# Performance work log

Measured on AMD Instinct MI355X. Metric: run time of the kernel, lower is better.

Reference implementation:

```python
import jax, jax.numpy as jnp
import numpy as np

B, C_IN, C_OUT, T, R, CO = 8, 64, 64, 32, 32, 32


def setup_inputs() -> dict:
    key = jax.random.key(0)
    ks = jax.random.split(key, 8)
    scale = 1.0 / np.sqrt(C_IN)  # nn.Linear default uniform(-1/sqrt(in), 1/sqrt(in))
    w = lambda k: jax.random.uniform(k, (C_OUT, C_IN), jnp.float32, -scale, scale)
    return {
        "x": jax.random.normal(ks[0], (B, C_IN, T, R, CO), jnp.float32),
        "w_self": w(ks[1]),
        "w_tp": w(ks[2]),
        "w_tm": w(ks[3]),
        "w_rp": w(ks[4]),
        "w_rm": w(ks[5]),
        "w_cp": w(ks[6]),
        "w_cm": w(ks[7]),
    }


def _proj(v, w):
    # v: [B, t, r, c, C_in], w: [C_out, C_in] (nn.Linear layout)
    return jnp.einsum('btrci,oi->btrco', v, w)


def _shift_pad(a, axis, front):
    # pad 1 slice at front (True) or back (False) along `axis` of a 5-D tensor
    pads = [(0, 0)] * 5
    pads[axis] = (1, 0) if front else (0, 1)
    return jnp.pad(a, pads)


def reference(x, w_self, w_tp, w_tm, w_rp, w_rm, w_cp, w_cm):
    xp = jnp.transpose(x, (0, 2, 3, 4, 1))  # [B, T, R, Co, C_in]
    out = _proj(xp, w_self)
    if xp.shape[1] > 1:
        out = out + _shift_pad(_proj(xp[:, :-1], w_tp), 1, True)
        out = out + _shift_pad(_proj(xp[:, 1:], w_tm), 1, False)
    if xp.shape[2] > 1:
        out = out + _shift_pad(_proj(xp[:, :, :-1], w_rp), 2, True)
        out = out + _shift_pad(_proj(xp[:, :, 1:], w_rm), 2, False)
    if xp.shape[3] > 1:
        out = out + _shift_pad(_proj(xp[:, :, :, :-1], w_cp), 3, True)
        out = out + _shift_pad(_proj(xp[:, :, :, 1:], w_cm), 3, False)
    return jnp.transpose(out, (0, 4, 1, 2, 3))  # [B, C_out, T, R, Co]
```

## Files before the change

### kernel.cpp

```cpp
#include <hip/hip_runtime.h>


#define SB 32768
#define CIN 64
#define COUT 64
#define NB 8

typedef short s16x8 __attribute__((ext_vector_type(8)));
typedef __bf16 bf16x8 __attribute__((ext_vector_type(8)));
typedef float f32x4 __attribute__((ext_vector_type(4)));

__device__ __forceinline__ unsigned f2bf(float f) {
    unsigned u = __float_as_uint(f);
    u += 0x7FFFu + ((u >> 16) & 1u);
    return u >> 16;
}
__device__ __forceinline__ unsigned pk2(float lo, float hi) {
    return f2bf(lo) | (f2bf(hi) << 16);
}

__global__ __launch_bounds__(256) void wprep_kernel(const float* __restrict__ w0,
                            const float* __restrict__ w1, const float* __restrict__ w2,
                            const float* __restrict__ w3, const float* __restrict__ w4,
                            const float* __restrict__ w5, const float* __restrict__ w6,
                            unsigned short* __restrict__ ws) {
    int tap = blockIdx.x;
    int tid = threadIdx.x;
    const float* w = (tap == 0) ? w0 : (tap == 1) ? w1 : (tap == 2) ? w2
                   : (tap == 3) ? w3 : (tap == 4) ? w4 : (tap == 5) ? w5 : w6;
    unsigned p[8];
#pragma unroll
    for (int j = 0; j < 8; ++j)
        p[j] = pk2(w[tid * 16 + 2 * j], w[tid * 16 + 2 * j + 1]);
    uint4* dp = (uint4*)(ws + tap * 4096 + tid * 16);
    dp[0] = make_uint4(p[0], p[1], p[2], p[3]);
    dp[1] = make_uint4(p[4], p[5], p[6], p[7]);
}

__global__ __launch_bounds__(256) void conv_kernel(const float* __restrict__ x,
                                                   const unsigned short* __restrict__ wq,
                                                   float* __restrict__ out) {
    __shared__ uint4 alds[2560];
    int bid = blockIdx.x;
    int b = bid >> 7;
    int sblk = (bid & 127) << 8;
    int tid = threadIdx.x;
    const float* xb = x + (size_t)b * CIN * SB;

    {
        int rl = 32 + tid;
        const float* xp = xb + sblk + tid;
#pragma unroll
        for (int c = 0; c < 4; ++c) {
            unsigned pk[8];
#pragma unroll
            for (int u = 0; u < 8; ++u)
                pk[u] = pk2(xp[(size_t)(c * 16 + 2 * u) * SB],
                            xp[(size_t)(c * 16 + 2 * u + 1) * SB]);
            alds[rl * 8 + ((2 * c) ^ (rl & 7))] = make_uint4(pk[0], pk[1], pk[2], pk[3]);
            alds[rl * 8 + ((2 * c + 1) ^ (rl & 7))] = make_uint4(pk[4], pk[5], pk[6], pk[7]);
        }
    }
    {
        int hrow = tid & 63;
        int rl = (hrow < 32) ? hrow : hrow + 256;
        int s = sblk - 32 + rl;
        s = max(0, min(SB - 1, s));
        int ic = tid >> 6;
        const float* xp = xb + s + (size_t)(ic * 16) * SB;
        unsigned pk[8];
#pragma unroll
        for (int u = 0; u < 8; ++u)
            pk[u] = pk2(xp[(size_t)(2 * u) * SB], xp[(size_t)(2 * u + 1) * SB]);
        alds[rl * 8 + ((2 * ic) ^ (rl & 7))] = make_uint4(pk[0], pk[1], pk[2], pk[3]);
        alds[rl * 8 + ((2 * ic + 1) ^ (rl & 7))] = make_uint4(pk[4], pk[5], pk[6], pk[7]);
    }
    __syncthreads();

    int lane = tid & 63;
    int wv = tid >> 6;
    int lo = lane & 15;
    int quad = lane >> 4;
    int sbase = sblk + wv * 64;
    int t = sblk >> 10;

    f32x4 acc[4][4];
#pragma unroll
    for (int mt = 0; mt < 4; ++mt)
#pragma unroll
        for (int nt = 0; nt < 4; ++nt)
            acc[mt][nt] = (f32x4){0.f, 0.f, 0.f, 0.f};

    int r_m[4], c_m[4], rl[4];
#pragma unroll
    for (int mt = 0; mt < 4; ++mt) {
        int s = sbase + mt * 16 + lo;
        r_m[mt] = (s >> 5) & 31;
        c_m[mt] = s & 31;
        rl[mt] = s - sblk + 32;
    }

    auto load_b = [&](const unsigned short* wt, int ks, int nt) -> bf16x8 {
        const unsigned short* bp = wt + (nt * 16 + lo) * 64 + ks * 32 + quad * 8;
        return __builtin_bit_cast(bf16x8, *(const s16x8*)bp);
    };

    auto run_tap_lds = [&](int tap, int d, const bool ok[4]) {
        const unsigned short* wt = wq + tap * 4096;
#pragma unroll
        for (int ks = 0; ks < 2; ++ks) {
            bf16x8 bf[4];
#pragma unroll
            for (int nt = 0; nt < 4; ++nt) bf[nt] = load_b(wt, ks, nt);
            int j = ks * 4 + quad;
#pragma unroll
            for (int mt = 0; mt < 4; ++mt) {
                int row = rl[mt] + d;
                s16x8 raw = *((const s16x8*)alds + row * 8 + (j ^ (row & 7)));
                s16x8 zz = {0, 0, 0, 0, 0, 0, 0, 0};
                raw = ok[mt] ? raw : zz;
                bf16x8 af = __builtin_bit_cast(bf16x8, raw);
#pragma unroll
                for (int nt = 0; nt < 4; ++nt)
                    acc[mt][nt] = __builtin_amdgcn_mfma_f32_16x16x32_bf16(af, bf[nt], acc[mt][nt], 0, 0, 0);
            }
        }
    };

    auto run_tap_gather = [&](int tap, int d) {
        const unsigned short* wt = wq + tap * 4096;
#pragma unroll
        for (int ks = 0; ks < 2; ++ks) {
            bf16x8 bf[4];
#pragma unroll
            for (int nt = 0; nt < 4; ++nt) bf[nt] = load_b(wt, ks, nt);
            const float* gp = xb + (size_t)(ks * 32 + quad * 8) * SB + d;
#pragma unroll
            for (int mt = 0; mt < 4; ++mt) {
                const float* ap = gp + sbase + mt * 16 + lo;
                unsigned pk[4];
#pragma unroll
                for (int u = 0; u < 4; ++u)
                    pk[u] = pk2(ap[(size_t)(2 * u) * SB], ap[(size_t)(2 * u + 1) * SB]);
                uint4 v = make_uint4(pk[0], pk[1], pk[2], pk[3]);
                bf16x8 af = __builtin_bit_cast(bf16x8, v);
#pragma unroll
                for (int nt = 0; nt < 4; ++nt)
                    acc[mt][nt] = __builtin_amdgcn_mfma_f32_16x16x32_bf16(af, bf[nt], acc[mt][nt], 0, 0, 0);
            }
        }
    };

    {
        bool ok_all[4] = {true, true, true, true};
        run_tap_lds(0, 0, ok_all);
    }
    if (t > 0)  run_tap_gather(1, -1024);
    if (t < 31) run_tap_gather(2, 1024);
    {
        bool ok[4];
#pragma unroll
        for (int mt = 0; mt < 4; ++mt) ok[mt] = (r_m[mt] > 0);
        run_tap_lds(3, -32, ok);
#pragma unroll
        for (int mt = 0; mt < 4; ++mt) ok[mt] = (r_m[mt] < 31);
        run_tap_lds(4, 32, ok);
#pragma unroll
        for (int mt = 0; mt < 4; ++mt) ok[mt] = (c_m[mt] > 0);
        run_tap_lds(5, -1, ok);
#pragma unroll
        for (int mt = 0; mt < 4; ++mt) ok[mt] = (c_m[mt] < 31);
        run_tap_lds(6, 1, ok);
    }

#pragma unroll
    for (int mt = 0; mt < 4; ++mt) {
#pragma unroll
        for (int nt = 0; nt < 4; ++nt) {
            int o = nt * 16 + lo;
            size_t off = ((size_t)(b * COUT + o)) * SB + sbase + mt * 16 + quad * 4;
            *(f32x4*)(out + off) = acc[mt][nt];
        }
    }
}

__global__ void fallback_kernel(const float* __restrict__ x,
                                const float* __restrict__ w0, const float* __restrict__ w1,
                                const float* __restrict__ w2, const float* __restrict__ w3,
                                const float* __restrict__ w4, const float* __restrict__ w5,
                                const float* __restrict__ w6,
                                float* __restrict__ out) {
    int bid = blockIdx.x;
    int b = bid >> 11;
    int og = (bid >> 7) & 15;
    int sblk = (bid & 127) << 8;
    int tid = threadIdx.x;
    __shared__ float wl[7][4][64];
    const float* wp[7] = {w0, w1, w2, w3, w4, w5, w6};
    for (int k = tid; k < 7 * 4 * 64; k += 256) {
        int tap = k >> 8, oo = (k >> 6) & 3, i = k & 63;
        wl[tap][oo][i] = wp[tap][(og * 4 + oo) * 64 + i];
    }
    __syncthreads();
    int s = sblk + tid;
    int t = s >> 10, r = (s >> 5) & 31, c = s & 31;
    const float* xb = x + (size_t)b * CIN * SB + s;
    float a0 = 0, a1 = 0, a2 = 0, a3 = 0;
    for (int i = 0; i < 64; ++i) {
        const float* xi = xb + (size_t)i * SB;
        float vs = xi[0];
        float vtp = (t > 0) ? xi[-1024] : 0.f;
        float vtm = (t < 31) ? xi[1024] : 0.f;
        float vrp = (r > 0) ? xi[-32] : 0.f;
        float vrm = (r < 31) ? xi[32] : 0.f;
        float vcp = (c > 0) ? xi[-1] : 0.f;
        float vcm = (c < 31) ? xi[1] : 0.f;
        a0 += wl[0][0][i] * vs + wl[1][0][i] * vtp + wl[2][0][i] * vtm + wl[3][0][i] * vrp + wl[4][0][i] * vrm + wl[5][0][i] * vcp + wl[6][0][i] * vcm;
        a1 += wl[0][1][i] * vs + wl[1][1][i] * vtp + wl[2][1][i] * vtm + wl[3][1][i] * vrp + wl[4][1][i] * vrm + wl[5][1][i] * vcp + wl[6][1][i] * vcm;
        a2 += wl[0][2][i] * vs + wl[1][2][i] * vtp + wl[2][2][i] * vtm + wl[3][2][i] * vrp + wl[4][2][i] * vrm + wl[5][2][i] * vcp + wl[6][2][i] * vcm;
        a3 += wl[0][3][i] * vs + wl[1][3][i] * vtp + wl[2][3][i] * vtm + wl[3][3][i] * vrp + wl[4][3][i] * vrm + wl[5][3][i] * vcp + wl[6][3][i] * vcm;
    }
    size_t obase = ((size_t)b * COUT + og * 4) * SB + s;
    out[obase] = a0;
    out[obase + SB] = a1;
    out[obase + 2 * (size_t)SB] = a2;
    out[obase + 3 * (size_t)SB] = a3;
}

extern "C" void kernel_launch(void* const* d_in, const int* in_sizes, int n_in,
                              void* d_out, int out_size, void* d_ws, size_t ws_size,
                              hipStream_t stream) {
    const float* x = (const float*)d_in[0];
    const float* w0 = (const float*)d_in[1];
    const float* w1 = (const float*)d_in[2];
    const float* w2 = (const float*)d_in[3];
    const float* w3 = (const float*)d_in[4];
    const float* w4 = (const float*)d_in[5];
    const float* w5 = (const float*)d_in[6];
    const float* w6 = (const float*)d_in[7];
    float* out = (float*)d_out;

    size_t need = (size_t)7 * 4096 * 2;
    if (d_ws != nullptr && ws_size >= need) {
        unsigned short* wsp = (unsigned short*)d_ws;
        wprep_kernel<<<7, 256, 0, stream>>>(w0, w1, w2, w3, w4, w5, w6, wsp);
        conv_kernel<<<1024, 256, 0, stream>>>(x, wsp, out);
    } else {
        fallback_kernel<<<8 * 16 * 128, 256, 0, stream>>>(x, w0, w1, w2, w3, w4, w5, w6, out);
    }
}
```

Measured before the change: 158.5 us.

## Stream T-slabs through an LDS ring with register-resident bf16 weights

Replaces the two-kernel scheme (weight prep plus per-256-position conv) with a single kernel. Each block covers one batch, a 32-position RC strip and 16 time steps, and streams x time slabs through a 4-deep LDS ring with two-step prefetch. The T-neighbour taps now read from adjacent ring slots instead of re-gathering x from global memory. All seven weight matrices are converted to bf16 in registers, and the launch drops to 512 blocks with a barrier per time step. This trades far less redundant global traffic and one fewer launch for higher register pressure, more sequential work per block and lower parallelism.

```diff
diff --git a/kernel.cpp b/kernel.cpp
--- a/kernel.cpp
+++ b/kernel.cpp
@@ -4,7 +4,6 @@
 #define SB 32768
 #define CIN 64
 #define COUT 64
-#define NB 8
 
 typedef short s16x8 __attribute__((ext_vector_type(8)));
 typedef __bf16 bf16x8 __attribute__((ext_vector_type(8)));
@@ -19,212 +18,149 @@
     return f2bf(lo) | (f2bf(hi) << 16);
 }
 
-__global__ __launch_bounds__(256) void wprep_kernel(const float* __restrict__ w0,
-                            const float* __restrict__ w1, const float* __restrict__ w2,
-                            const float* __restrict__ w3, const float* __restrict__ w4,
-                            const float* __restrict__ w5, const float* __restrict__ w6,
-                            unsigned short* __restrict__ ws) {
-    int tap = blockIdx.x;
+__global__ __launch_bounds__(256) void conv11_kernel(const float* __restrict__ x,
+        const float* __restrict__ w0, const float* __restrict__ w1,
+        const float* __restrict__ w2, const float* __restrict__ w3,
+        const float* __restrict__ w4, const float* __restrict__ w5,
+        const float* __restrict__ w6, float* __restrict__ out) {
+    __shared__ uint4 ring[4][768];
+    int bid = blockIdx.x;
+    int b = bid & 7;
+    int rc0 = ((bid >> 3) & 31) << 5;
+    int t0 = (bid >> 8) << 4;
     int tid = threadIdx.x;
-    const float* w = (tap == 0) ? w0 : (tap == 1) ? w1 : (tap == 2) ? w2
-                   : (tap == 3) ? w3 : (tap == 4) ? w4 : (tap == 5) ? w5 : w6;
-    unsigned p[8];
-#pragma unroll
-    for (int j = 0; j < 8; ++j)
-        p[j] = pk2(w[tid * 16 + 2 * j], w[tid * 16 + 2 * j + 1]);
-    uint4* dp = (uint4*)(ws + tap * 4096 + tid * 16);
-    dp[0] = make_uint4(p[0], p[1], p[2], p[3]);
-    dp[1] = make_uint4(p[4], p[5], p[6], p[7]);
-}
-
-__global__ __launch_bounds__(256) void conv_kernel(const float* __restrict__ x,
-                                                   const unsigned short* __restrict__ wq,
-                                                   float* __restrict__ out) {
-    __shared__ uint4 alds[2560];
-    int bid = blockIdx.x;
-    int b = bid >> 7;
-    int sblk = (bid & 127) << 8;
-    int tid = threadIdx.x;
-    const float* xb = x + (size_t)b * CIN * SB;
-
-    {
-        int rl = 32 + tid;
-        const float* xp = xb + sblk + tid;
-#pragma unroll
-        for (int c = 0; c < 4; ++c) {
-            unsigned pk[8];
-#pragma unroll
-            for (int u = 0; u < 8; ++u)
-                pk[u] = pk2(xp[(size_t)(c * 16 + 2 * u) * SB],
-                            xp[(size_t)(c * 16 + 2 * u + 1) * SB]);
-            alds[rl * 8 + ((2 * c) ^ (rl & 7))] = make_uint4(pk[0], pk[1], pk[2], pk[3]);
-            alds[rl * 8 + ((2 * c + 1) ^ (rl & 7))] = make_uint4(pk[4], pk[5], pk[6], pk[7]);
-        }
-    }
-    {
-        int hrow = tid & 63;
-        int rl = (hrow < 32) ? hrow : hrow + 256;
-        int s = sblk - 32 + rl;
-        s = max(0, min(SB - 1, s));
-        int ic = tid >> 6;
-        const float* xp = xb + s + (size_t)(ic * 16) * SB;
-        unsigned pk[8];
-#pragma unroll
-        for (int u = 0; u < 8; ++u)
-            pk[u] = pk2(xp[(size_t)(2 * u) * SB], xp[(size_t)(2 * u + 1) * SB]);
-        alds[rl * 8 + ((2 * ic) ^ (rl & 7))] = make_uint4(pk[0], pk[1], pk[2], pk[3]);
-        alds[rl * 8 + ((2 * ic + 1) ^ (rl & 7))] = make_uint4(pk[4], pk[5], pk[6], pk[7]);
-    }
-    __syncthreads();
-
     int lane = tid & 63;
     int wv = tid >> 6;
     int lo = lane & 15;
     int quad = lane >> 4;
-    int sbase = sblk + wv * 64;
-    int t = sblk >> 10;
+    int oh = wv & 1;
+    int rh = wv >> 1;
+    const float* xb = x + (size_t)b * CIN * SB;
 
-    f32x4 acc[4][4];
+    const float* wp[7] = {w0, w1, w2, w3, w4, w5, w6};
+    bf16x8 bq[7][2][2];
 #pragma unroll
-    for (int mt = 0; mt < 4; ++mt)
+    for (int tap = 0; tap < 7; ++tap)
 #pragma unroll
-        for (int nt = 0; nt < 4; ++nt)
-            acc[mt][nt] = (f32x4){0.f, 0.f, 0.f, 0.f};
+        for (int ks = 0; ks < 2; ++ks)
+#pragma unroll
+            for (int nt = 0; nt < 2; ++nt) {
+                const float* p = wp[tap] + (oh * 32 + nt * 16 + lo) * 64 + ks * 32 + quad * 8;
+                float4 f0 = *(const float4*)p;
+                float4 f1 = *(const float4*)(p + 4);
+                uint4 v = make_uint4(pk2(f0.x, f0.y), pk2(f0.z, f0.w),
+                                     pk2(f1.x, f1.y), pk2(f1.z, f1.w));
+                bq[tap][ks][nt] = __builtin_bit_cast(bf16x8, v);
+            }
 
-    int r_m[4], c_m[4], rl[4];
+    int rc = rc0 + rh * 16 + lo;
+    int rl = 32 + rh * 16 + lo;
+    int r = rc >> 5;
+    int c = rc & 31;
+    bool okrm = (r > 0), okrp = (r < 31), okcm = (c > 0), okcp = (c < 31);
+
+    int cg1 = tid & 7, s21 = tid >> 3;
+    int rx1 = rc0 - 32 + 2 * s21;
+    rx1 = rx1 < 0 ? 0 : (rx1 > 1022 ? 1022 : rx1);
+    int cg2 = tid & 7, s22 = 32 + (tid >> 3);
+    int rx2 = rc0 - 32 + 2 * s22;
+    rx2 = rx2 > 1022 ? 1022 : rx2;
+
+    float2 va[8], vb[8];
+    auto stage_load = [&](int ts) {
+        const float* g1 = xb + (size_t)(cg1 * 8) * SB + ts * 1024 + rx1;
 #pragma unroll
-    for (int mt = 0; mt < 4; ++mt) {
-        int s = sbase + mt * 16 + lo;
-        r_m[mt] = (s >> 5) & 31;
-        c_m[mt] = s & 31;
-        rl[mt] = s - sblk + 32;
-    }
-
-    auto load_b = [&](const unsigned short* wt, int ks, int nt) -> bf16x8 {
-        const unsigned short* bp = wt + (nt * 16 + lo) * 64 + ks * 32 + quad * 8;
-        return __builtin_bit_cast(bf16x8, *(const s16x8*)bp);
-    };
-
-    auto run_tap_lds = [&](int tap, int d, const bool ok[4]) {
-        const unsigned short* wt = wq + tap * 4096;
+        for (int u = 0; u < 4; ++u) {
+            va[u]     = *(const float2*)(g1 + (size_t)(2 * u) * SB);
+            va[u + 4] = *(const float2*)(g1 + (size_t)(2 * u + 1) * SB);
+        }
+        if (tid < 128) {
+            const float* g2 = xb + (size_t)(cg2 * 8) * SB + ts * 1024 + rx2;
 #pragma unroll
-        for (int ks = 0; ks < 2; ++ks) {
-            bf16x8 bf[4];
-#pragma unroll
-            for (int nt = 0; nt < 4; ++nt) bf[nt] = load_b(wt, ks, nt);
-            int j = ks * 4 + quad;
-#pragma unroll
-            for (int mt = 0; mt < 4; ++mt) {
-                int row = rl[mt] + d;
-                s16x8 raw = *((const s16x8*)alds + row * 8 + (j ^ (row & 7)));
-                s16x8 zz = {0, 0, 0, 0, 0, 0, 0, 0};
-                raw = ok[mt] ? raw : zz;
-                bf16x8 af = __builtin_bit_cast(bf16x8, raw);
-#pragma unroll
-                for (int nt = 0; nt < 4; ++nt)
-                    acc[mt][nt] = __builtin_amdgcn_mfma_f32_16x16x32_bf16(af, bf[nt], acc[mt][nt], 0, 0, 0);
+            for (int u = 0; u < 4; ++u) {
+                vb[u]     = *(const float2*)(g2 + (size_t)(2 * u) * SB);
+                vb[u + 4] = *(const float2*)(g2 + (size_t)(2 * u + 1) * SB);
             }
         }
     };
-
-    auto run_tap_gather = [&](int tap, int d) {
-        const unsigned short* wt = wq + tap * 4096;
-#pragma unroll
-        for (int ks = 0; ks < 2; ++ks) {
-            bf16x8 bf[4];
-#pragma unroll
-            for (int nt = 0; nt < 4; ++nt) bf[nt] = load_b(wt, ks, nt);
-            const float* gp = xb + (size_t)(ks * 32 + quad * 8) * SB + d;
-#pragma unroll
-            for (int mt = 0; mt < 4; ++mt) {
-                const float* ap = gp + sbase + mt * 16 + lo;
-                unsigned pk[4];
-#pragma unroll
-                for (int u = 0; u < 4; ++u)
-                    pk[u] = pk2(ap[(size_t)(2 * u) * SB], ap[(size_t)(2 * u + 1) * SB]);
-                uint4 v = make_uint4(pk[0], pk[1], pk[2], pk[3]);
-                bf16x8 af = __builtin_bit_cast(bf16x8, v);
-#pragma unroll
-                for (int nt = 0; nt < 4; ++nt)
-                    acc[mt][nt] = __builtin_amdgcn_mfma_f32_16x16x32_bf16(af, bf[nt], acc[mt][nt], 0, 0, 0);
-            }
+    auto stage_write = [&](int ts) {
+        int k = ts & 3;
+        {
+            int rw = 2 * s21;
+            uint4 A = make_uint4(pk2(va[0].x, va[4].x), pk2(va[1].x, va[5].x),
+                                 pk2(va[2].x, va[6].x), pk2(va[3].x, va[7].x));
+            uint4 B = make_uint4(pk2(va[0].y, va[4].y), pk2(va[1].y, va[5].y),
+                                 pk2(va[2].y, va[6].y), pk2(va[3].y, va[7].y));
+            ring[k][rw * 8 + (cg1 ^ (rw & 7))] = A;
+            ring[k][(rw + 1) * 8 + (cg1 ^ ((rw + 1) & 7))] = B;
+        }
+        if (tid < 128) {
+            int rw = 2 * s22;
+            uint4 A = make_uint4(pk2(vb[0].x, vb[4].x), pk2(vb[1].x, vb[5].x),
+                                 pk2(vb[2].x, vb[6].x), pk2(vb[3].x, vb[7].x));
+            uint4 B = make_uint4(pk2(vb[0].y, vb[4].y), pk2(vb[1].y, vb[5].y),
+                                 pk2(vb[2].y, vb[6].y), pk2(vb[3].y, vb[7].y));
+            ring[k][rw * 8 + (cg2 ^ (rw & 7))] = A;
+            ring[k][(rw + 1) * 8 + (cg2 ^ ((rw + 1) & 7))] = B;
         }
     };
 
-    {
-        bool ok_all[4] = {true, true, true, true};
-        run_tap_lds(0, 0, ok_all);
+    const s16x8 zz = {0, 0, 0, 0, 0, 0, 0, 0};
+    f32x4 aA0, aB0, aA1, aB1;
+
+    auto tap_f = [&](const uint4* slab, const bf16x8 (&bt)[2][2], int d, bool ok) {
+        int row = rl + d;
+        s16x8 a0 = *((const s16x8*)slab + row * 8 + (quad ^ (row & 7)));
+        s16x8 a1 = *((const s16x8*)slab + row * 8 + ((4 + quad) ^ (row & 7)));
+        a0 = ok ? a0 : zz;
+        a1 = ok ? a1 : zz;
+        bf16x8 af0 = __builtin_bit_cast(bf16x8, a0);
+        bf16x8 af1 = __builtin_bit_cast(bf16x8, a1);
+        aA0 = __builtin_amdgcn_mfma_f32_16x16x32_bf16(af0, bt[0][0], aA0, 0, 0, 0);
+        aB0 = __builtin_amdgcn_mfma_f32_16x16x32_bf16(af1, bt[1][0], aB0, 0, 0, 0);
+        aA1 = __builtin_amdgcn_mfma_f32_16x16x32_bf16(af0, bt[0][1], aA1, 0, 0, 0);
+        aB1 = __builtin_amdgcn_mfma_f32_16x16x32_bf16(af1, bt[1][1], aB1, 0, 0, 0);
+    };
+
+    if (t0 > 0) { stage_load(t0 - 1); stage_write(t0 - 1); }
+    stage_load(t0);     stage_write(t0);
+    stage_load(t0 + 1); stage_write(t0 + 1);
+    asm volatile("s_waitcnt lgkmcnt(0)" ::: "memory");
+    __builtin_amdgcn_s_barrier();
+    __builtin_amdgcn_sched_barrier(0);
+
+    int smax = (t0 == 0) ? 16 : 31;
+    for (int t = t0; t < t0 + 16; ++t) {
+        bool pf = (t + 2 <= smax);
+        if (pf) stage_load(t + 2);
+
+        aA0 = (f32x4){0.f, 0.f, 0.f, 0.f};
+        aB0 = (f32x4){0.f, 0.f, 0.f, 0.f};
+        aA1 = (f32x4){0.f, 0.f, 0.f, 0.f};
+        aB1 = (f32x4){0.f, 0.f, 0.f, 0.f};
+        const uint4* s0 = &ring[t & 3][0];
+
+        tap_f(s0, bq[0], 0, true);
+        if (t > 0)  tap_f(&ring[(t - 1) & 3][0], bq[1], 0, true);
+        if (t < 31) tap_f(&ring[(t + 1) & 3][0], bq[2], 0, true);
+        tap_f(s0, bq[3], -32, okrm);
+        tap_f(s0, bq[4], 32, okrp);
+        tap_f(s0, bq[5], -1, okcm);
+        tap_f(s0, bq[6], 1, okcp);
+
+        f32x4 o0 = aA0 + aB0;
+        f32x4 o1 = aA1 + aB1;
+        size_t ob = ((size_t)(b * COUT + oh * 32 + lo)) * SB
+                  + (size_t)t * 1024 + rc0 + rh * 16 + quad * 4;
+        *(f32x4*)(out + ob) = o0;
+        *(f32x4*)(out + ob + (size_t)16 * SB) = o1;
+
+        if (pf) stage_write(t + 2);
+
+        asm volatile("s_waitcnt lgkmcnt(0)" ::: "memory");
+        __builtin_amdgcn_s_barrier();
+        __builtin_amdgcn_sched_barrier(0);
     }
-    if (t > 0)  run_tap_gather(1, -1024);
-    if (t < 31) run_tap_gather(2, 1024);
-    {
-        bool ok[4];
-#pragma unroll
-        for (int mt = 0; mt < 4; ++mt) ok[mt] = (r_m[mt] > 0);
-        run_tap_lds(3, -32, ok);
-#pragma unroll
-        for (int mt = 0; mt < 4; ++mt) ok[mt] = (r_m[mt] < 31);
-        run_tap_lds(4, 32, ok);
-#pragma unroll
-        for (int mt = 0; mt < 4; ++mt) ok[mt] = (c_m[mt] > 0);
-        run_tap_lds(5, -1, ok);
-#pragma unroll
-        for (int mt = 0; mt < 4; ++mt) ok[mt] = (c_m[mt] < 31);
-        run_tap_lds(6, 1, ok);
-    }
-
-#pragma unroll
-    for (int mt = 0; mt < 4; ++mt) {
-#pragma unroll
-        for (int nt = 0; nt < 4; ++nt) {
-            int o = nt * 16 + lo;
-            size_t off = ((size_t)(b * COUT + o)) * SB + sbase + mt * 16 + quad * 4;
-            *(f32x4*)(out + off) = acc[mt][nt];
-        }
-    }
-}
-
-__global__ void fallback_kernel(const float* __restrict__ x,
-                                const float* __restrict__ w0, const float* __restrict__ w1,
-                                const float* __restrict__ w2, const float* __restrict__ w3,
-                                const float* __restrict__ w4, const float* __restrict__ w5,
-                                const float* __restrict__ w6,
-                                float* __restrict__ out) {
-    int bid = blockIdx.x;
-    int b = bid >> 11;
-    int og = (bid >> 7) & 15;
-    int sblk = (bid & 127) << 8;
-    int tid = threadIdx.x;
-    __shared__ float wl[7][4][64];
-    const float* wp[7] = {w0, w1, w2, w3, w4, w5, w6};
-    for (int k = tid; k < 7 * 4 * 64; k += 256) {
-        int tap = k >> 8, oo = (k >> 6) & 3, i = k & 63;
-        wl[tap][oo][i] = wp[tap][(og * 4 + oo) * 64 + i];
-    }
-    __syncthreads();
-    int s = sblk + tid;
-    int t = s >> 10, r = (s >> 5) & 31, c = s & 31;
-    const float* xb = x + (size_t)b * CIN * SB + s;
-    float a0 = 0, a1 = 0, a2 = 0, a3 = 0;
-    for (int i = 0; i < 64; ++i) {
-        const float* xi = xb + (size_t)i * SB;
-        float vs = xi[0];
-        float vtp = (t > 0) ? xi[-1024] : 0.f;
-        float vtm = (t < 31) ? xi[1024] : 0.f;
-        float vrp = (r > 0) ? xi[-32] : 0.f;
-        float vrm = (r < 31) ? xi[32] : 0.f;
-        float vcp = (c > 0) ? xi[-1] : 0.f;
-        float vcm = (c < 31) ? xi[1] : 0.f;
-        a0 += wl[0][0][i] * vs + wl[1][0][i] * vtp + wl[2][0][i] * vtm + wl[3][0][i] * vrp + wl[4][0][i] * vrm + wl[5][0][i] * vcp + wl[6][0][i] * vcm;
-        a1 += wl[0][1][i] * vs + wl[1][1][i] * vtp + wl[2][1][i] * vtm + wl[3][1][i] * vrp + wl[4][1][i] * vrm + wl[5][1][i] * vcp + wl[6][1][i] * vcm;
-        a2 += wl[0][2][i] * vs + wl[1][2][i] * vtp + wl[2][2][i] * vtm + wl[3][2][i] * vrp + wl[4][2][i] * vrm + wl[5][2][i] * vcp + wl[6][2][i] * vcm;
-        a3 += wl[0][3][i] * vs + wl[1][3][i] * vtp + wl[2][3][i] * vtm + wl[3][3][i] * vrp + wl[4][3][i] * vrm + wl[5][3][i] * vcp + wl[6][3][i] * vcm;
-    }
-    size_t obase = ((size_t)b * COUT + og * 4) * SB + s;
-    out[obase] = a0;
-    out[obase + SB] = a1;
-    out[obase + 2 * (size_t)SB] = a2;
-    out[obase + 3 * (size_t)SB] = a3;
 }
 
 extern "C" void kernel_launch(void* const* d_in, const int* in_sizes, int n_in,
@@ -239,13 +175,7 @@
     const float* w5 = (const float*)d_in[6];
     const float* w6 = (const float*)d_in[7];
     float* out = (float*)d_out;
+    (void)d_ws; (void)ws_size;
 
-    size_t need = (size_t)7 * 4096 * 2;
-    if (d_ws != nullptr && ws_size >= need) {
-        unsigned short* wsp = (unsigned short*)d_ws;
-        wprep_kernel<<<7, 256, 0, stream>>>(w0, w1, w2, w3, w4, w5, w6, wsp);
-        conv_kernel<<<1024, 256, 0, stream>>>(x, wsp, out);
-    } else {
-        fallback_kernel<<<8 * 16 * 128, 256, 0, stream>>>(x, w0, w1, w2, w3, w4, w5, w6, out);
-    }
+    conv11_kernel<<<512, 256, 0, stream>>>(x, w0, w1, w2, w3, w4, w5, w6, out);
 }
```

Result: slower. 193.1 us (+21.9%).
